# Kernel tuning notes

Hardware: AMD Instinct MI355X
Metric: run time of the kernel (lower is better)

## Reference

```python
import jax, jax.numpy as jnp
import numpy as np

VOCAB = 1_000_000
DIM = 64
BATCH = 16384
BAG = 50


def setup_inputs() -> dict:
    key = jax.random.key(0)
    k_idx, k_w, k_emb = jax.random.split(key, 3)
    indices = jax.random.randint(k_idx, (BATCH, BAG), 0, VOCAB, dtype=jnp.int64 if jax.config.jax_enable_x64 else jnp.int32)
    weights = jax.random.uniform(k_w, (BATCH, BAG), dtype=jnp.float32)
    values = jax.random.normal(k_emb, (VOCAB, DIM), dtype=jnp.float32)
    return {"indices": indices, "weights": weights, "values": values}


def reference(indices, weights, values):
    # Fused gather + weighted sum: out[b, d] = sum_n weights[b, n] * values[indices[b, n], d]
    gathered = jnp.take(values, indices, axis=0)  # [B, BAG, D]
    return jnp.einsum("bn,bnd->bd", weights, gathered)
```

## Files before the change

### kernel.cpp

```cpp
#include <hip/hip_runtime.h>

#define BATCH 16384
#define BAG   50
#define DIM   64

__global__ __launch_bounds__(256) void embag_kernel(
    const int*   __restrict__ indices,
    const float* __restrict__ weights,
    const float* __restrict__ values,
    float*       __restrict__ out)
{
    const int gtid = blockIdx.x * blockDim.x + threadIdx.x;
    const int bag  = gtid >> 6;
    const int lane = threadIdx.x & 63;
    if (bag >= BATCH) return;

    int   my_idx = 0;
    float my_w   = 0.0f;
    if (lane < BAG) {
        my_idx = indices[bag * BAG + lane];
        my_w   = weights[bag * BAG + lane];
    }

    float acc = 0.0f;
    #pragma unroll
    for (int n = 0; n < BAG; ++n) {
        const int   idx = __shfl(my_idx, n, 64);
        const float w   = __shfl(my_w,   n, 64);
        acc += w * values[(long long)idx * DIM + lane];
    }

    out[bag * DIM + lane] = acc;
}

extern "C" void kernel_launch(void* const* d_in, const int* in_sizes, int n_in,
                              void* d_out, int out_size, void* d_ws, size_t ws_size,
                              hipStream_t stream) {
    const int*   indices = (const int*)  d_in[0];
    const float* weights = (const float*)d_in[1];
    const float* values  = (const float*)d_in[2];
    float*       out     = (float*)      d_out;

    const int waves_per_block = 4;
    const int blocks = (BATCH + waves_per_block - 1) / waves_per_block;
    embag_kernel<<<blocks, 256, 0, stream>>>(indices, weights, values, out);
}
```

Baseline: 36.76 us.

## Split bag rows across four quarter-waves with float4 gathers and shuffle reduction

Each wave now divides its bag's 50 rows among four 16-lane groups. Every lane loads a float4 slice of a row, so each group gathers a full 256-byte row per instruction, and the group partial sums are combined with xor shuffles. Indices and weights are loaded straight into registers, which removes the per-row broadcast shuffles. This cuts the number of dependent load instructions per wave and exposes more memory parallelism, at the cost of extra registers and a reduction step, and only a quarter of the lanes do the store.

```diff
diff --git a/kernel.cpp b/kernel.cpp
--- a/kernel.cpp
+++ b/kernel.cpp
@@ -3,6 +3,7 @@
 #define BATCH 16384
 #define BAG   50
 #define DIM   64
+#define NT    13
 
 __global__ __launch_bounds__(256) void embag_kernel(
     const int*   __restrict__ indices,
@@ -13,24 +14,43 @@
     const int gtid = blockIdx.x * blockDim.x + threadIdx.x;
     const int bag  = gtid >> 6;
     const int lane = threadIdx.x & 63;
+    const int sub  = lane >> 4;
+    const int li   = lane & 15;
     if (bag >= BATCH) return;
 
-    int   my_idx = 0;
-    float my_w   = 0.0f;
-    if (lane < BAG) {
-        my_idx = indices[bag * BAG + lane];
-        my_w   = weights[bag * BAG + lane];
+    int   idxs[NT];
+    float ws[NT];
+    #pragma unroll
+    for (int t = 0; t < NT; ++t) {
+        const int nn = t * 4 + sub;
+        const bool ok = nn < BAG;
+        idxs[t] = ok ? indices[bag * BAG + nn] : 0;
+        ws[t]   = ok ? weights[bag * BAG + nn] : 0.0f;
     }
 
-    float acc = 0.0f;
+    float4 acc = make_float4(0.f, 0.f, 0.f, 0.f);
     #pragma unroll
-    for (int n = 0; n < BAG; ++n) {
-        const int   idx = __shfl(my_idx, n, 64);
-        const float w   = __shfl(my_w,   n, 64);
-        acc += w * values[(long long)idx * DIM + lane];
+    for (int t = 0; t < NT; ++t) {
+        const float4 v = *reinterpret_cast<const float4*>(
+            &values[(long long)idxs[t] * DIM + li * 4]);
+        const float w = ws[t];
+        acc.x += w * v.x;
+        acc.y += w * v.y;
+        acc.z += w * v.z;
+        acc.w += w * v.w;
     }
 
-    out[bag * DIM + lane] = acc;
+    #pragma unroll
+    for (int m = 16; m <= 32; m <<= 1) {
+        acc.x += __shfl_xor(acc.x, m, 64);
+        acc.y += __shfl_xor(acc.y, m, 64);
+        acc.z += __shfl_xor(acc.z, m, 64);
+        acc.w += __shfl_xor(acc.w, m, 64);
+    }
+
+    if (sub == 0) {
+        *reinterpret_cast<float4*>(&out[bag * DIM + li * 4]) = acc;
+    }
 }
 
 extern "C" void kernel_launch(void* const* d_in, const int* in_sizes, int n_in,
```

New measurement: 36.22 us. Within noise of the previous version (-1.5%).
